# Performance work log

Hardware: AMD Instinct MI355X
Metric: run time of the kernel (lower is better)

## Reference

```python
import jax, jax.numpy as jnp
import numpy as np

H, W = 256, 256
N = 1024          # gaussians
G = 2             # num_gabor
RANK = 6          # abundance channels / endmembers
C = 128           # spectral bands
LORA_ALPHA = 0.1


def setup_inputs() -> dict:
    key = jax.random.key(0)
    ks = jax.random.split(key, 8)
    xyz = 0.5 * jax.random.normal(ks[0], (N, 2), jnp.float32)          # pre-tanh means
    cholesky = jnp.zeros((N, 3), jnp.float32)                           # + bound -> identity-ish cov
    feat0 = jnp.log(jnp.expm1(jnp.float32(0.05)))                       # inverse softplus(0.05)
    features_dc = feat0 + 0.01 * jax.random.normal(ks[1], (N, RANK), jnp.float32)
    gabor_freqs = (jax.random.uniform(ks[2], (N * G, 2), jnp.float32) - 0.5) * 0.002
    gabor_weights = jax.random.uniform(ks[3], (N * G, 1), jnp.float32) * -5.0
    lora_U = 0.3 * jax.random.normal(ks[4], (RANK, 2), jnp.float32)
    lora_V = 0.001 * jax.random.normal(ks[5], (2, C), jnp.float32)
    lora_scale_logit = jnp.zeros((1,), jnp.float32)
    opacity = jnp.ones((N, 1), jnp.float32)
    endmember = jax.random.uniform(ks[6], (RANK, C), jnp.float32)
    return {"xyz": xyz, "cholesky": cholesky, "features_dc": features_dc,
            "gabor_freqs": gabor_freqs, "gabor_weights": gabor_weights,
            "lora_U": lora_U, "lora_V": lora_V, "lora_scale_logit": lora_scale_logit,
            "opacity": opacity, "endmember": endmember}


def _rasterize_gabor_sum(xyz, cholesky, features_dc, gabor_freqs, gabor_weights, opacity):
    # project_gaussians_2d: tanh means in [-1,1] -> pixel coords
    means = jnp.tanh(xyz)                                               # [N,2]
    centers = (means * 0.5 + 0.5) * jnp.array([W, H], jnp.float32)      # [N,2] (x,y)
    ch = cholesky + jnp.array([0.5, 0.0, 0.5], jnp.float32)             # cholesky bound
    l1, l2, l3 = ch[:, 0], ch[:, 1], ch[:, 2]
    # Sigma = L L^T, L = [[l1,0],[l2,l3]] -> conic = Sigma^{-1}
    a = l1 * l1
    b = l1 * l2
    c = l2 * l2 + l3 * l3
    det = a * c - b * b
    ca, cb, cc = c / det, -b / det, a / det                             # [N]
    # pixel grid, row-major flat index p = y*W + x, pixel centers at +0.5
    xs = jnp.arange(W, dtype=jnp.float32) + 0.5
    ys = jnp.arange(H, dtype=jnp.float32) + 0.5
    px = jnp.tile(xs, H)                                                # [HW]
    py = jnp.repeat(ys, W)                                              # [HW]
    dx = px[None, :] - centers[:, 0:1]                                  # [N,HW]
    dy = py[None, :] - centers[:, 1:2]                                  # [N,HW]
    sigma = 0.5 * (ca[:, None] * dx * dx + cc[:, None] * dy * dy) + cb[:, None] * dx * dy
    gauss = jnp.where(sigma >= 0, jnp.exp(-sigma), 0.0)                 # [N,HW]
    # gabor modulation: 1 + sum_g w_g * cos(fx_g*dx + fy_g*dy)
    fx = jnp.exp(gabor_freqs[:, 0]).reshape(N, G)
    fy = jnp.exp(gabor_freqs[:, 1]).reshape(N, G)
    gw = jax.nn.sigmoid(gabor_weights[:, 0]).reshape(N, G)
    mod = jnp.ones_like(gauss)
    for g in range(G):  # small fixed loop over gabor components
        mod = mod + gw[:, g:g + 1] * jnp.cos(fx[:, g:g + 1] * dx + fy[:, g:g + 1] * dy)
    wmat = gauss * mod                                                  # [N,HW]
    feats = jax.nn.softplus(features_dc) * opacity                      # [N,RANK]
    # sum-blending rasterization (background = 0); linear in features so
    # the 3/4-channel group split in the original concatenates to the same result
    abundance = jnp.einsum('np,nr->pr', wmat, feats)                    # [HW,RANK]
    return jnp.maximum(abundance, 0.0)


def reference(xyz, cholesky, features_dc, gabor_freqs, gabor_weights,
              lora_U, lora_V, lora_scale_logit, opacity, endmember):
    abundance = _rasterize_gabor_sum(xyz, cholesky, features_dc,
                                     gabor_freqs, gabor_weights, opacity)
    # LoRA-calibrated endmember
    delta = jnp.tanh(lora_U @ lora_V)                                   # [RANK,C]
    scale = LORA_ALPHA * jnp.tanh(lora_scale_logit[0])
    E = jnp.clip(endmember + scale * delta, 1e-6, None)
    render = (abundance @ E).reshape(1, H, W, C).transpose(0, 3, 1, 2)  # [1,C,H,W]
    return render, abundance, E
```

## Files before the change

### kernel.cpp

```cpp
#include <hip/hip_runtime.h>
#include <math.h>

#define HH 256
#define WW 256
#define NPTS 1024
#define RANK 6
#define NC 128
#define PIX (HH * WW)
#define SIGMA_CUT 18.0f
#define PSTRIDE 20
#define MAXG 256
#define TPAD 264

typedef float vf4 __attribute__((ext_vector_type(4)));

__device__ __forceinline__ float softplus_f(float x) {
    return fmaxf(x, 0.0f) + log1pf(__expf(-fabsf(x)));
}

__global__ __launch_bounds__(256) void fused_kernel(
    const float* __restrict__ xyz, const float* __restrict__ chol,
    const float* __restrict__ fdc, const float* __restrict__ gfreq,
    const float* __restrict__ gwt, const float* __restrict__ opac,
    const float* __restrict__ lU, const float* __restrict__ lV,
    const float* __restrict__ lS, const float* __restrict__ em,
    float* __restrict__ render, float* __restrict__ abund,
    float* __restrict__ Eout)
{
    __shared__ float Els[64 * 8];
    __shared__ float glist[MAXG * PSTRIDE];
    __shared__ int   idxl[MAXG];
    __shared__ int   wcnt[4];
    __shared__ float accT[RANK * TPAD];

    const int t    = threadIdx.x;
    const int bid  = blockIdx.x;
    const int cg   = bid & 1;
    const int tile = bid >> 1;
    const int tx   = (tile & 3) * 64;
    const int ty   = (tile >> 2) * 4;
    const int x    = tx + (t & 63);
    const int y    = ty + (t >> 6);
    const float px = (float)x + 0.5f;
    const float py = (float)y + 0.5f;
    const int wv   = t >> 6;
    const int ln   = t & 63;

    {
        float scale = 0.1f * tanhf(lS[0]);
        for (int i = t; i < 64 * RANK; i += 256) {
            int r = i >> 6; int cl = i & 63; int c = cg * 64 + cl;
            float dot = lU[r * 2] * lV[c] + lU[r * 2 + 1] * lV[NC + c];
            Els[cl * 8 + r] = fmaxf(em[r * NC + c] + scale * tanhf(dot), 1e-6f);
        }
        if (bid == 0) {
            for (int i = t; i < RANK * NC; i += 256) {
                int r = i >> 7; int c = i & 127;
                float dot = lU[r * 2] * lV[c] + lU[r * 2 + 1] * lV[NC + c];
                Eout[i] = fmaxf(em[i] + scale * tanhf(dot), 1e-6f);
            }
        }
    }

    const float txmin = (float)tx, txmax = (float)(tx + 64);
    const float tymin = (float)ty, tymax = (float)(ty + 4);
    int total = 0;
    for (int k = 0; k < 4; ++k) {
        const int gid = k * 256 + t;
        float cx = (tanhf(xyz[gid * 2 + 0]) * 0.5f + 0.5f) * (float)WW;
        float cy = (tanhf(xyz[gid * 2 + 1]) * 0.5f + 0.5f) * (float)HH;
        float l1 = chol[gid * 3 + 0] + 0.5f;
        float l2 = chol[gid * 3 + 1];
        float l3 = chol[gid * 3 + 2] + 0.5f;
        float a = l1 * l1;
        float c = l2 * l2 + l3 * l3;
        float rx = 6.0f * sqrtf(a);
        float ry = 6.0f * sqrtf(c);
        bool hit = (cx - rx <= txmax) && (cx + rx >= txmin) &&
                   (cy - ry <= tymax) && (cy + ry >= tymin);
        unsigned long long m = __ballot(hit);
        if (ln == 0) wcnt[wv] = __popcll(m);
        __syncthreads();
        int base = total;
        for (int w = 0; w < 4; ++w) { if (w < wv) base += wcnt[w]; }
        total += wcnt[0] + wcnt[1] + wcnt[2] + wcnt[3];
        if (hit) {
            int pos = base + __popcll(m & ((1ull << ln) - 1ull));
            if (pos < MAXG) idxl[pos] = gid;
        }
        __syncthreads();
    }
    const int T = min(total, MAXG);

    for (int j = t; j < T; j += 256) {
        const int n = idxl[j];
        float cx = (tanhf(xyz[n * 2 + 0]) * 0.5f + 0.5f) * (float)WW;
        float cy = (tanhf(xyz[n * 2 + 1]) * 0.5f + 0.5f) * (float)HH;
        float l1 = chol[n * 3 + 0] + 0.5f;
        float l2 = chol[n * 3 + 1];
        float l3 = chol[n * 3 + 2] + 0.5f;
        float a = l1 * l1, bb = l1 * l2, c = l2 * l2 + l3 * l3;
        float inv = 1.0f / (a * c - bb * bb);
        float* g = glist + j * PSTRIDE;
        g[0] = cx; g[1] = cy;
        g[2] = c * inv; g[3] = -bb * inv; g[4] = a * inv;
        g[5] = __expf(gfreq[n * 4 + 0]);
        g[6] = __expf(gfreq[n * 4 + 1]);
        g[7] = __expf(gfreq[n * 4 + 2]);
        g[8] = __expf(gfreq[n * 4 + 3]);
        g[9]  = 1.0f / (1.0f + __expf(-gwt[n * 2 + 0]));
        g[10] = 1.0f / (1.0f + __expf(-gwt[n * 2 + 1]));
        float op = opac[n];
#pragma unroll
        for (int r = 0; r < RANK; ++r)
            g[11 + r] = softplus_f(fdc[n * RANK + r]) * op;
    }
    __syncthreads();

    float acc[RANK] = {0.f, 0.f, 0.f, 0.f, 0.f, 0.f};
    for (int i = 0; i < T; ++i) {
        const vf4* gv = (const vf4*)(glist + i * PSTRIDE);
        vf4 g0 = gv[0];
        vf4 g1 = gv[1];
        vf4 g2 = gv[2];
        float dx = px - g0.x;
        float dy = py - g0.y;
        float sigma = 0.5f * (g0.z * dx * dx + g1.x * dy * dy) + g0.w * dx * dy;
        if (sigma < 0.0f || sigma > SIGMA_CUT) continue;
        vf4 g3 = gv[3];
        vf4 g4 = gv[4];
        float wm = __expf(-sigma) *
                   (1.0f + g2.y * __cosf(g1.y * dx + g1.z * dy)
                         + g2.z * __cosf(g1.w * dx + g2.x * dy));
        acc[0] = fmaf(wm, g2.w, acc[0]);
        acc[1] = fmaf(wm, g3.x, acc[1]);
        acc[2] = fmaf(wm, g3.y, acc[2]);
        acc[3] = fmaf(wm, g3.z, acc[3]);
        acc[4] = fmaf(wm, g3.w, acc[4]);
        acc[5] = fmaf(wm, g4.x, acc[5]);
    }
#pragma unroll
    for (int r = 0; r < RANK; ++r) acc[r] = fmaxf(acc[r], 0.0f);

#pragma unroll
    for (int r = 0; r < RANK; ++r)
        accT[r * TPAD + t] = acc[r];
    __syncthreads();

    const int u    = t & 63;
    const int wv2  = t >> 6;
    const int row  = (u >> 4);
    const int xg   = (u & 15);
    const int p0   = (ty + row) * WW + tx + xg * 4;

    vf4 ab[RANK];
#pragma unroll
    for (int r = 0; r < RANK; ++r)
        ab[r] = *(const vf4*)(accT + r * TPAD + 4 * u);

    if (cg == 0 && wv2 == 0) {
        vf4* ao = (vf4*)(abund + (size_t)p0 * RANK);
        vf4 o0 = { ab[0][0], ab[1][0], ab[2][0], ab[3][0] };
        vf4 o1 = { ab[4][0], ab[5][0], ab[0][1], ab[1][1] };
        vf4 o2 = { ab[2][1], ab[3][1], ab[4][1], ab[5][1] };
        vf4 o3 = { ab[0][2], ab[1][2], ab[2][2], ab[3][2] };
        vf4 o4 = { ab[4][2], ab[5][2], ab[0][3], ab[1][3] };
        vf4 o5 = { ab[2][3], ab[3][3], ab[4][3], ab[5][3] };
        __builtin_nontemporal_store(o0, ao + 0);
        __builtin_nontemporal_store(o1, ao + 1);
        __builtin_nontemporal_store(o2, ao + 2);
        __builtin_nontemporal_store(o3, ao + 3);
        __builtin_nontemporal_store(o4, ao + 4);
        __builtin_nontemporal_store(o5, ao + 5);
    }

    float* rp = render + (size_t)cg * 64 * PIX + p0;
#pragma unroll
    for (int i = 0; i < 16; ++i) {
        const int cl = wv2 * 16 + i;
        const vf4 e0 = *(const vf4*)(Els + cl * 8);
        const vf4 e1 = *(const vf4*)(Els + cl * 8 + 4);
        vf4 o = ab[0] * e0.x;
        o += ab[1] * e0.y;
        o += ab[2] * e0.z;
        o += ab[3] * e0.w;
        o += ab[4] * e1.x;
        o += ab[5] * e1.y;
        __builtin_nontemporal_store(o, (vf4*)(rp + (size_t)cl * PIX));
    }
}

extern "C" void kernel_launch(void* const* d_in, const int* in_sizes, int n_in,
                              void* d_out, int out_size, void* d_ws, size_t ws_size,
                              hipStream_t stream)
{
    const float* xyz             = (const float*)d_in[0];
    const float* cholesky        = (const float*)d_in[1];
    const float* features_dc     = (const float*)d_in[2];
    const float* gabor_freqs     = (const float*)d_in[3];
    const float* gabor_weights   = (const float*)d_in[4];
    const float* lora_U          = (const float*)d_in[5];
    const float* lora_V          = (const float*)d_in[6];
    const float* lora_scale_logit= (const float*)d_in[7];
    const float* opacity         = (const float*)d_in[8];
    const float* endmember       = (const float*)d_in[9];

    float* out    = (float*)d_out;
    float* render = out;
    float* abund  = out + (size_t)NC * PIX;
    float* Eout   = abund + (size_t)PIX * RANK;

    fused_kernel<<<512, 256, 0, stream>>>(
        xyz, cholesky, features_dc, gabor_freqs, gabor_weights, opacity,
        lora_U, lora_V, lora_scale_logit, endmember, render, abund, Eout);
}
```

Baseline: 20.54 us.

## Split channels into four groups, per-wave culling lists, branchless gaussian loop

Each tile now runs as four blocks of 32 output channels instead of two blocks of 64, doubling the grid to 1024 blocks so more work is in flight for the store-bound render output. Culling now has each wave build its own segment list with a single barrier, replacing the four barrier-synchronised block-wide compaction rounds. The per-pixel loop drops the sigma>18 early-out and masks negative sigma with a select, removing divergent branches. In exchange, every gaussian evaluation is recomputed by twice as many blocks, and the order of the gaussian list changes.

After: 21.74 us. 5.8% more time.

```diff
diff --git a/kernel.cpp b/kernel.cpp
--- a/kernel.cpp
+++ b/kernel.cpp
@@ -7,9 +7,11 @@
 #define RANK 6
 #define NC 128
 #define PIX (HH * WW)
-#define SIGMA_CUT 18.0f
+#define CGRP 4
+#define CHB (NC / CGRP)
 #define PSTRIDE 20
 #define MAXG 256
+#define SEG 128
 #define TPAD 264
 
 typedef float vf4 __attribute__((ext_vector_type(4)));
@@ -27,29 +29,27 @@
     float* __restrict__ render, float* __restrict__ abund,
     float* __restrict__ Eout)
 {
-    __shared__ float Els[64 * 8];
+    __shared__ float Els[CHB * 8];
     __shared__ float glist[MAXG * PSTRIDE];
-    __shared__ int   idxl[MAXG];
+    __shared__ int   idxl[4 * SEG];
     __shared__ int   wcnt[4];
     __shared__ float accT[RANK * TPAD];
 
     const int t    = threadIdx.x;
     const int bid  = blockIdx.x;
-    const int cg   = bid & 1;
-    const int tile = bid >> 1;
+    const int cg   = bid & 3;
+    const int tile = bid >> 2;
     const int tx   = (tile & 3) * 64;
     const int ty   = (tile >> 2) * 4;
-    const int x    = tx + (t & 63);
-    const int y    = ty + (t >> 6);
-    const float px = (float)x + 0.5f;
-    const float py = (float)y + 0.5f;
+    const float px = (float)(tx + (t & 63)) + 0.5f;
+    const float py = (float)(ty + (t >> 6)) + 0.5f;
     const int wv   = t >> 6;
     const int ln   = t & 63;
 
     {
         float scale = 0.1f * tanhf(lS[0]);
-        for (int i = t; i < 64 * RANK; i += 256) {
-            int r = i >> 6; int cl = i & 63; int c = cg * 64 + cl;
+        if (t < CHB * RANK) {
+            int r = t >> 5; int cl = t & 31; int c = cg * CHB + cl;
             float dot = lU[r * 2] * lV[c] + lU[r * 2 + 1] * lV[NC + c];
             Els[cl * 8 + r] = fmaxf(em[r * NC + c] + scale * tanhf(dot), 1e-6f);
         }
@@ -64,36 +64,45 @@
 
     const float txmin = (float)tx, txmax = (float)(tx + 64);
     const float tymin = (float)ty, tymax = (float)(ty + 4);
-    int total = 0;
-    for (int k = 0; k < 4; ++k) {
-        const int gid = k * 256 + t;
-        float cx = (tanhf(xyz[gid * 2 + 0]) * 0.5f + 0.5f) * (float)WW;
-        float cy = (tanhf(xyz[gid * 2 + 1]) * 0.5f + 0.5f) * (float)HH;
-        float l1 = chol[gid * 3 + 0] + 0.5f;
-        float l2 = chol[gid * 3 + 1];
-        float l3 = chol[gid * 3 + 2] + 0.5f;
-        float a = l1 * l1;
-        float c = l2 * l2 + l3 * l3;
-        float rx = 6.0f * sqrtf(a);
-        float ry = 6.0f * sqrtf(c);
-        bool hit = (cx - rx <= txmax) && (cx + rx >= txmin) &&
-                   (cy - ry <= tymax) && (cy + ry >= tymin);
-        unsigned long long m = __ballot(hit);
-        if (ln == 0) wcnt[wv] = __popcll(m);
-        __syncthreads();
-        int base = total;
-        for (int w = 0; w < 4; ++w) { if (w < wv) base += wcnt[w]; }
-        total += wcnt[0] + wcnt[1] + wcnt[2] + wcnt[3];
-        if (hit) {
-            int pos = base + __popcll(m & ((1ull << ln) - 1ull));
-            if (pos < MAXG) idxl[pos] = gid;
+    {
+        int cnt = 0;
+        const int gbase = wv * 256;
+        for (int k = 0; k < 4; ++k) {
+            const int gid = gbase + k * 64 + ln;
+            float cx = (tanhf(xyz[gid * 2 + 0]) * 0.5f + 0.5f) * (float)WW;
+            float cy = (tanhf(xyz[gid * 2 + 1]) * 0.5f + 0.5f) * (float)HH;
+            float l1 = chol[gid * 3 + 0] + 0.5f;
+            float l2 = chol[gid * 3 + 1];
+            float l3 = chol[gid * 3 + 2] + 0.5f;
+            float a = l1 * l1;
+            float c = l2 * l2 + l3 * l3;
+            float rx = 6.0f * sqrtf(a);
+            float ry = 6.0f * sqrtf(c);
+            bool hit = (cx - rx <= txmax) && (cx + rx >= txmin) &&
+                       (cy - ry <= tymax) && (cy + ry >= tymin);
+            unsigned long long m = __ballot(hit);
+            if (hit) {
+                int pos = cnt + __popcll(m & ((1ull << ln) - 1ull));
+                if (pos < SEG) idxl[wv * SEG + pos] = gid;
+            }
+            cnt += __popcll(m);
         }
-        __syncthreads();
-    }
-    const int T = min(total, MAXG);
+        if (ln == 0) wcnt[wv] = min(cnt, SEG);
+    }
+    __syncthreads();
+
+    const int c0 = wcnt[0], c1 = wcnt[1], c2 = wcnt[2], c3 = wcnt[3];
+    const int o1 = c0, o2 = c0 + c1, o3 = o2 + c2;
+    int T = o3 + c3;
+    if (T > MAXG) T = MAXG;
 
     for (int j = t; j < T; j += 256) {
-        const int n = idxl[j];
+        int w, o;
+        if (j < o1)      { w = 0; o = j; }
+        else if (j < o2) { w = 1; o = j - o1; }
+        else if (j < o3) { w = 2; o = j - o2; }
+        else             { w = 3; o = j - o3; }
+        const int n = idxl[w * SEG + o];
         float cx = (tanhf(xyz[n * 2 + 0]) * 0.5f + 0.5f) * (float)WW;
         float cy = (tanhf(xyz[n * 2 + 1]) * 0.5f + 0.5f) * (float)HH;
         float l1 = chol[n * 3 + 0] + 0.5f;
@@ -126,12 +135,12 @@
         float dx = px - g0.x;
         float dy = py - g0.y;
         float sigma = 0.5f * (g0.z * dx * dx + g1.x * dy * dy) + g0.w * dx * dy;
-        if (sigma < 0.0f || sigma > SIGMA_CUT) continue;
         vf4 g3 = gv[3];
         vf4 g4 = gv[4];
         float wm = __expf(-sigma) *
                    (1.0f + g2.y * __cosf(g1.y * dx + g1.z * dy)
                          + g2.z * __cosf(g1.w * dx + g2.x * dy));
+        wm = (sigma >= 0.0f) ? wm : 0.0f;
         acc[0] = fmaf(wm, g2.w, acc[0]);
         acc[1] = fmaf(wm, g3.x, acc[1]);
         acc[2] = fmaf(wm, g3.y, acc[2]);
@@ -147,11 +156,11 @@
         accT[r * TPAD + t] = acc[r];
     __syncthreads();
 
-    const int u    = t & 63;
-    const int wv2  = t >> 6;
-    const int row  = (u >> 4);
-    const int xg   = (u & 15);
-    const int p0   = (ty + row) * WW + tx + xg * 4;
+    const int u   = t & 63;
+    const int wv2 = t >> 6;
+    const int row = u >> 4;
+    const int xg  = u & 15;
+    const int p0  = (ty + row) * WW + tx + xg * 4;
 
     vf4 ab[RANK];
 #pragma unroll
@@ -160,24 +169,24 @@
 
     if (cg == 0 && wv2 == 0) {
         vf4* ao = (vf4*)(abund + (size_t)p0 * RANK);
-        vf4 o0 = { ab[0][0], ab[1][0], ab[2][0], ab[3][0] };
-        vf4 o1 = { ab[4][0], ab[5][0], ab[0][1], ab[1][1] };
-        vf4 o2 = { ab[2][1], ab[3][1], ab[4][1], ab[5][1] };
-        vf4 o3 = { ab[0][2], ab[1][2], ab[2][2], ab[3][2] };
-        vf4 o4 = { ab[4][2], ab[5][2], ab[0][3], ab[1][3] };
-        vf4 o5 = { ab[2][3], ab[3][3], ab[4][3], ab[5][3] };
-        __builtin_nontemporal_store(o0, ao + 0);
-        __builtin_nontemporal_store(o1, ao + 1);
-        __builtin_nontemporal_store(o2, ao + 2);
-        __builtin_nontemporal_store(o3, ao + 3);
-        __builtin_nontemporal_store(o4, ao + 4);
-        __builtin_nontemporal_store(o5, ao + 5);
-    }
-
-    float* rp = render + (size_t)cg * 64 * PIX + p0;
-#pragma unroll
-    for (int i = 0; i < 16; ++i) {
-        const int cl = wv2 * 16 + i;
+        vf4 q0 = { ab[0][0], ab[1][0], ab[2][0], ab[3][0] };
+        vf4 q1 = { ab[4][0], ab[5][0], ab[0][1], ab[1][1] };
+        vf4 q2 = { ab[2][1], ab[3][1], ab[4][1], ab[5][1] };
+        vf4 q3 = { ab[0][2], ab[1][2], ab[2][2], ab[3][2] };
+        vf4 q4 = { ab[4][2], ab[5][2], ab[0][3], ab[1][3] };
+        vf4 q5 = { ab[2][3], ab[3][3], ab[4][3], ab[5][3] };
+        __builtin_nontemporal_store(q0, ao + 0);
+        __builtin_nontemporal_store(q1, ao + 1);
+        __builtin_nontemporal_store(q2, ao + 2);
+        __builtin_nontemporal_store(q3, ao + 3);
+        __builtin_nontemporal_store(q4, ao + 4);
+        __builtin_nontemporal_store(q5, ao + 5);
+    }
+
+    float* rp = render + (size_t)cg * CHB * PIX + p0;
+#pragma unroll
+    for (int i = 0; i < CHB / 4; ++i) {
+        const int cl = wv2 * (CHB / 4) + i;
         const vf4 e0 = *(const vf4*)(Els + cl * 8);
         const vf4 e1 = *(const vf4*)(Els + cl * 8 + 4);
         vf4 o = ab[0] * e0.x;
@@ -210,7 +219,7 @@
     float* abund  = out + (size_t)NC * PIX;
     float* Eout   = abund + (size_t)PIX * RANK;
 
-    fused_kernel<<<512, 256, 0, stream>>>(
+    fused_kernel<<<1024, 256, 0, stream>>>(
         xyz, cholesky, features_dc, gabor_freqs, gabor_weights, opacity,
         lora_U, lora_V, lora_scale_logit, endmember, render, abund, Eout);
 }
```
